# Kernel tuning notes

Measured on AMD Instinct MI355X. Metric: run time of the kernel, lower is better.

Reference implementation:

```python
import jax, jax.numpy as jnp
import numpy as np

D = 1024
HEADS = 16
LN_EPS = 1e-5   # torch LayerNorm default
SHEP_EPS = 1e-4 # eps in shepards_MHA
SHEP_P = 2


def setup_inputs() -> dict:
    key = jax.random.key(0)
    k1, k2, k3 = jax.random.split(key, 3)
    b, t, d = 2, 2048, D
    X = jax.random.normal(k1, (b, t, d), dtype=jnp.float32)
    # Linear weights, scaled like torch default init (~U(-1/sqrt(fan_in), ...)) magnitude
    W_in = jax.random.normal(k2, (4 * d, d), dtype=jnp.float32) * (1.0 / np.sqrt(d))
    b_in = jnp.zeros((4 * d,), dtype=jnp.float32)
    W_out = jax.random.normal(k3, (d, d), dtype=jnp.float32) * (1.0 / np.sqrt(d))
    b_out = jnp.zeros((d,), dtype=jnp.float32)
    return {"X": X, "W_in": W_in, "b_in": b_in, "W_out": W_out, "b_out": b_out}


def _shepards_mha(Q, K, V):
    # Q,K,V: [b,h,t,dh]. Euclidean cdist via ||q||^2 + ||k||^2 - 2 q.k
    q2 = jnp.sum(Q * Q, axis=-1, keepdims=True)          # [b,h,t,1]
    k2 = jnp.sum(K * K, axis=-1, keepdims=True)          # [b,h,t,1]
    sq = q2 + jnp.swapaxes(k2, -1, -2) - 2.0 * jnp.einsum('bhqd,bhkd->bhqk', Q, K)
    dist = jnp.sqrt(jnp.maximum(sq, 0.0))                # [b,h,t,t]
    W = (SHEP_EPS + dist) ** (-SHEP_P)
    W = W / (SHEP_EPS + jnp.sum(W, axis=-1, keepdims=True))
    return jnp.einsum('bhqk,bhkd->bhqd', W, V)


def reference(X, W_in, b_in, W_out, b_out):
    b, t, d = X.shape
    h = HEADS
    dh = d // h
    # LayerNorm (no affine)
    mu = jnp.mean(X, axis=-1, keepdims=True)
    var = jnp.mean((X - mu) ** 2, axis=-1, keepdims=True)
    Xn = (X - mu) / jnp.sqrt(var + LN_EPS)
    # project_in: [b,t,4d]
    P = jnp.einsum('btd,ed->bte', Xn, W_in) + b_in
    # [b,t,h,4*dh] -> [b,h,t,4*dh]
    P = P.reshape(b, t, h, 4 * dh).transpose(0, 2, 1, 3)
    Q, K, V, G = jnp.split(P, 4, axis=-1)                # each [b,h,t,dh]
    A = _shepards_mha(Q, K, V)
    O = (G * A).transpose(0, 2, 1, 3).reshape(b, t, d)
    return X + jnp.einsum('btd,ed->bte', O, W_out) + b_out
```

## Files before the change

kernel.cpp:

```cpp
#include <hip/hip_runtime.h>

#define SEQ 2048
#define D_MODEL 1024
#define NTOK 4096
#define PROW 4096
#define DH 64
#define LN_EPS 1e-5f
#define SHEP_EPS 1e-4f

typedef __attribute__((ext_vector_type(8))) short bf16x8;
typedef __attribute__((ext_vector_type(4))) short s16x4;
typedef __attribute__((ext_vector_type(4))) float f32x4;

__device__ __forceinline__ unsigned short f2bf(float f) {
  union { float f; unsigned u; } v; v.f = f;
  unsigned r = v.u + 0x7fffu + ((v.u >> 16) & 1u);
  return (unsigned short)(r >> 16);
}
__device__ __forceinline__ float bf2f(unsigned short s) {
  union { unsigned u; float f; } v; v.u = ((unsigned)s) << 16;
  return v.f;
}
__device__ __forceinline__ void gload16(const void* g, void* l) {
  __builtin_amdgcn_global_load_lds(
      (const __attribute__((address_space(1))) unsigned int*)g,
      (__attribute__((address_space(3))) unsigned int*)l, 16, 0, 0);
}
__device__ __forceinline__ void gload4(const void* g, void* l) {
  __builtin_amdgcn_global_load_lds(
      (const __attribute__((address_space(1))) unsigned int*)g,
      (__attribute__((address_space(3))) unsigned int*)l, 4, 0, 0);
}
__device__ __forceinline__ unsigned cvt_pk_bf16(float lo, float hi) {
  unsigned r;
  asm("v_cvt_pk_bf16_f32 %0, %1, %2" : "=v"(r) : "v"(lo), "v"(hi));
  return r;
}
#define MFMA16(a, b, c) __builtin_amdgcn_mfma_f32_16x16x32_bf16(a, b, c, 0, 0, 0)

__global__ __launch_bounds__(256) void ln_kernel(const float* __restrict__ X,
                                                 unsigned short* __restrict__ Xn) {
  int row = blockIdx.x, tid = threadIdx.x;
  const float4* xr = (const float4*)(X + (size_t)row * D_MODEL);
  float4 v = xr[tid];
  float s = v.x + v.y + v.z + v.w;
  float s2 = v.x * v.x + v.y * v.y + v.z * v.z + v.w * v.w;
#pragma unroll
  for (int off = 32; off > 0; off >>= 1) {
    s += __shfl_down(s, off);
    s2 += __shfl_down(s2, off);
  }
  __shared__ float red[8];
  __shared__ float mb[2];
  int wv = tid >> 6;
  if ((tid & 63) == 0) { red[wv] = s; red[4 + wv] = s2; }
  __syncthreads();
  if (tid == 0) {
    float ts = red[0] + red[1] + red[2] + red[3];
    float t2 = red[4] + red[5] + red[6] + red[7];
    float mu = ts * (1.f / D_MODEL);
    float var = t2 * (1.f / D_MODEL) - mu * mu;
    mb[0] = mu;
    mb[1] = rsqrtf(var + LN_EPS);
  }
  __syncthreads();
  float mu = mb[0], rs = mb[1];
  s16x4 o;
  o[0] = (short)f2bf((v.x - mu) * rs);
  o[1] = (short)f2bf((v.y - mu) * rs);
  o[2] = (short)f2bf((v.z - mu) * rs);
  o[3] = (short)f2bf((v.w - mu) * rs);
  ((s16x4*)(Xn + (size_t)row * D_MODEL))[tid] = o;
}

__global__ __launch_bounds__(256) void cvt_bf16_kernel(const float* __restrict__ in,
                                                       unsigned short* __restrict__ out,
                                                       int n4) {
  int i = blockIdx.x * 256 + threadIdx.x;
  if (i >= n4) return;
  float4 v = ((const float4*)in)[i];
  s16x4 o;
  o[0] = (short)f2bf(v.x);
  o[1] = (short)f2bf(v.y);
  o[2] = (short)f2bf(v.z);
  o[3] = (short)f2bf(v.w);
  ((s16x4*)out)[i] = o;
}

__global__ __launch_bounds__(256) void gemm_p_kernel(
    const unsigned short* __restrict__ A, const unsigned short* __restrict__ B,
    const float* __restrict__ bias, unsigned short* __restrict__ C,
    int M, int N, int K) {
  __shared__ __align__(16) unsigned short sA[128 * 32];
  __shared__ __align__(16) unsigned short sB[128 * 32];
  int tid = threadIdx.x;
  int m0 = blockIdx.y * 128, n0 = blockIdx.x * 128;
  int wv = tid >> 6, lane = tid & 63;
  int wr = wv >> 1, wc = wv & 1;
  int lr = lane & 15, lq = lane >> 4;
  f32x4 acc[4][4] = {};
  int srow = tid >> 2, scol = (tid & 3) * 8;
  const unsigned short* gA = A + (size_t)(m0 + srow) * K + scol;
  const unsigned short* gB = B + (size_t)(n0 + srow) * K + scol;
  unsigned short* lA = sA + tid * 8;
  unsigned short* lB = sB + tid * 8;
  for (int k0 = 0; k0 < K; k0 += 32) {
    gload16(gA + k0, lA);
    gload16(gA + k0 + (size_t)64 * K, lA + 64 * 32);
    gload16(gB + k0, lB);
    gload16(gB + k0 + (size_t)64 * K, lB + 64 * 32);
    __syncthreads();
    bf16x8 af[4], bfr[4];
#pragma unroll
    for (int m = 0; m < 4; m++)
      af[m] = *(const bf16x8*)&sA[(wr * 64 + m * 16 + lr) * 32 + lq * 8];
#pragma unroll
    for (int n = 0; n < 4; n++)
      bfr[n] = *(const bf16x8*)&sB[(wc * 64 + n * 16 + lr) * 32 + lq * 8];
#pragma unroll
    for (int m = 0; m < 4; m++)
#pragma unroll
      for (int n = 0; n < 4; n++)
        acc[m][n] = MFMA16(af[m], bfr[n], acc[m][n]);
    __syncthreads();
  }
#pragma unroll
  for (int m = 0; m < 4; m++) {
    int row = m0 + wr * 64 + m * 16 + lq * 4;
#pragma unroll
    for (int n = 0; n < 4; n++) {
      int col = n0 + wc * 64 + n * 16 + lr;
      float bv = bias[col];
#pragma unroll
      for (int r = 0; r < 4; r++)
        C[(size_t)(row + r) * N + col] = f2bf(acc[m][n][r] + bv);
    }
  }
}

__global__ __launch_bounds__(256) void gemm_out_kernel(
    const unsigned short* __restrict__ A, const unsigned short* __restrict__ B,
    const float* __restrict__ bias, const float* __restrict__ Xres,
    float* __restrict__ Out, int M, int N, int K) {
  __shared__ __align__(16) unsigned short sA[128 * 32];
  __shared__ __align__(16) unsigned short sB[128 * 32];
  int tid = threadIdx.x;
  int m0 = blockIdx.y * 128, n0 = blockIdx.x * 128;
  int wv = tid >> 6, lane = tid & 63;
  int wr = wv >> 1, wc = wv & 1;
  int lr = lane & 15, lq = lane >> 4;
  f32x4 acc[4][4] = {};
  int srow = tid >> 2, scol = (tid & 3) * 8;
  const unsigned short* gA = A + (size_t)(m0 + srow) * K + scol;
  const unsigned short* gB = B + (size_t)(n0 + srow) * K + scol;
  unsigned short* lA = sA + tid * 8;
  unsigned short* lB = sB + tid * 8;
  for (int k0 = 0; k0 < K; k0 += 32) {
    gload16(gA + k0, lA);
    gload16(gA + k0 + (size_t)64 * K, lA + 64 * 32);
    gload16(gB + k0, lB);
    gload16(gB + k0 + (size_t)64 * K, lB + 64 * 32);
    __syncthreads();
    bf16x8 af[4], bfr[4];
#pragma unroll
    for (int m = 0; m < 4; m++)
      af[m] = *(const bf16x8*)&sA[(wr * 64 + m * 16 + lr) * 32 + lq * 8];
#pragma unroll
    for (int n = 0; n < 4; n++)
      bfr[n] = *(const bf16x8*)&sB[(wc * 64 + n * 16 + lr) * 32 + lq * 8];
#pragma unroll
    for (int m = 0; m < 4; m++)
#pragma unroll
      for (int n = 0; n < 4; n++)
        acc[m][n] = MFMA16(af[m], bfr[n], acc[m][n]);
    __syncthreads();
  }
#pragma unroll
  for (int m = 0; m < 4; m++) {
    int row = m0 + wr * 64 + m * 16 + lq * 4;
#pragma unroll
    for (int n = 0; n < 4; n++) {
      int col = n0 + wc * 64 + n * 16 + lr;
      float bv = bias[col];
#pragma unroll
      for (int r = 0; r < 4; r++) {
        size_t idx = (size_t)(row + r) * N + col;
        Out[idx] = Xres[idx] + acc[m][n][r] + bv;
      }
    }
  }
}

__global__ __launch_bounds__(256) void transv_kernel(const unsigned short* __restrict__ P,
                                                     unsigned short* __restrict__ Vt) {
  int kt = blockIdx.x;
  int bh = blockIdx.y;
  int b = bh >> 4, h = bh & 15;
  __shared__ unsigned short sT[64][72];
  int tid = threadIdx.x;
  const unsigned short* vbase = P + ((size_t)(b * SEQ + kt * 64)) * PROW + h * 256 + 128;
#pragma unroll
  for (int it = 0; it < 2; it++) {
    int c = tid + it * 256;
    int k = c >> 3, c0 = (c & 7) * 8;
    uint4 u = *(const uint4*)(vbase + (size_t)k * PROW + c0);
    unsigned e[4] = {u.x, u.y, u.z, u.w};
#pragma unroll
    for (int j = 0; j < 4; j++) {
      sT[c0 + 2 * j][k] = (unsigned short)(e[j] & 0xffffu);
      sT[c0 + 2 * j + 1][k] = (unsigned short)(e[j] >> 16);
    }
  }
  __syncthreads();
  unsigned short* obase = Vt + (size_t)bh * 64 * SEQ + kt * 64;
#pragma unroll
  for (int it = 0; it < 2; it++) {
    int cc = tid + it * 256;
    int crow = cc >> 3, k0 = (cc & 7) * 8;
    uint4 o;
    unsigned short e[8];
#pragma unroll
    for (int j = 0; j < 8; j++) e[j] = sT[crow][k0 + j];
    o.x = (unsigned)e[0] | ((unsigned)e[1] << 16);
    o.y = (unsigned)e[2] | ((unsigned)e[3] << 16);
    o.z = (unsigned)e[4] | ((unsigned)e[5] << 16);
    o.w = (unsigned)e[6] | ((unsigned)e[7] << 16);
    *(uint4*)(obase + (size_t)crow * SEQ + k0) = o;
  }
}

__global__ __launch_bounds__(256) void norms_kernel(const unsigned short* __restrict__ P,
                                                    float* __restrict__ nrm) {
  int id = blockIdx.x * 256 + threadIdx.x;
  int bh = id >> 12;
  int which = (id >> 11) & 1;
  int t = id & 2047;
  int b = bh >> 4, h = bh & 15;
  const unsigned short* p = P + ((size_t)(b * SEQ + t)) * PROW + h * 256 + which * 64;
  const uint4* pv = (const uint4*)p;
  float acc = 0.f;
#pragma unroll
  for (int i = 0; i < 8; i++) {
    uint4 u = pv[i];
    unsigned arr[4] = {u.x, u.y, u.z, u.w};
#pragma unroll
    for (int j = 0; j < 4; j++) {
      float lo = __uint_as_float(arr[j] << 16);
      float hi = __uint_as_float(arr[j] & 0xffff0000u);
      acc += lo * lo + hi * hi;
    }
  }
  nrm[(size_t)(bh * 2 + which) * SEQ + t] = acc;
}

__global__ __launch_bounds__(512) void attn_kernel(
    const unsigned short* __restrict__ P, const unsigned short* __restrict__ Vt,
    const float* __restrict__ nrm, unsigned short* __restrict__ O) {
  int qt = blockIdx.x, bh = blockIdx.y;
  int b = bh >> 4, h = bh & 15;
  int tid = threadIdx.x;
  int w = tid >> 6, lane = tid & 63;
  int lr = lane & 15, lq = lane >> 4;

  __shared__ __align__(16) unsigned short sQ[128 * 64];
  __shared__ __align__(16) unsigned short sK[2][64 * 64];
  __shared__ __align__(16) unsigned short sV[2][64 * 64];
  __shared__ __align__(16) unsigned short sW[128 * 64];
  __shared__ __align__(16) float sK2[2][64];
  __shared__ __align__(16) float sDen[8][16];

  const unsigned short* qbase = P + ((size_t)(b * SEQ + qt * 128)) * PROW + h * 256;
  const unsigned short* kbase = P + ((size_t)(b * SEQ)) * PROW + h * 256 + 64;
  const unsigned short* vtb = Vt + (size_t)bh * 64 * SEQ;
  const float* k2base = nrm + (size_t)(bh * 2 + 1) * SEQ;

  int srow = tid >> 3;
  int scol = ((tid & 7) ^ (srow & 7)) * 8;
  const unsigned short* kSrc = kbase + (size_t)srow * PROW + scol;
  const unsigned short* vSrc = vtb + (size_t)srow * SEQ + scol;

#pragma unroll
  for (int it = 0; it < 2; it++) {
    int c = tid + it * 512;
    int row = c >> 3;
    int col = ((c & 7) ^ (row & 7)) * 8;
    gload16(qbase + (size_t)row * PROW + col, (char*)sQ + c * 16);
  }
  gload16(kSrc, (char*)&sK[0][0] + tid * 16);
  gload16(vSrc, (char*)&sV[0][0] + tid * 16);
  if (w == 0) gload4(k2base + lane, (char*)&sK2[0][0] + lane * 4);
  float q2 = nrm[(size_t)(bh * 2) * SEQ + qt * 128 + 16 * w + lr];
  __syncthreads();

  int qrow = 16 * w + lr;
  bf16x8 qf[2];
#pragma unroll
  for (int ks = 0; ks < 2; ks++)
    qf[ks] = *(const bf16x8*)((const char*)sQ + qrow * 128 +
                              ((ks * 64 + lq * 16) ^ ((lr & 7) << 4)));

  f32x4 num[4] = {};
  float den = 0.f;
  char* wrow = (char*)sW + qrow * 128;

  for (int kt = 0; kt < SEQ / 64; kt++) {
    int cur = kt & 1, nxt = cur ^ 1;
    if (kt < SEQ / 64 - 1) {
      gload16(kSrc + (size_t)(kt + 1) * 64 * PROW, (char*)&sK[nxt][0] + tid * 16);
      gload16(vSrc + (size_t)(kt + 1) * 64, (char*)&sV[nxt][0] + tid * 16);
      if (w == 0) gload4(k2base + (kt + 1) * 64 + lane, (char*)&sK2[nxt][0] + lane * 4);
    }

    f32x4 st[4] = {};
#pragma unroll
    for (int fk = 0; fk < 4; fk++) {
      int row = 16 * fk + lr;
      const char* krow = (const char*)&sK[cur][0] + row * 128;
      bf16x8 kf0 = *(const bf16x8*)(krow + ((lq * 16) ^ ((row & 7) << 4)));
      bf16x8 kf1 = *(const bf16x8*)(krow + ((64 + lq * 16) ^ ((row & 7) << 4)));
      st[fk] = MFMA16(kf0, qf[0], st[fk]);
      st[fk] = MFMA16(kf1, qf[1], st[fk]);
    }

#pragma unroll
    for (int fk = 0; fk < 4; fk++) {
      f32x4 k2v = *(const f32x4*)&sK2[cur][16 * fk + 4 * lq];
      float w0 = __builtin_amdgcn_rcpf(fmaxf(fmaf(-2.f, st[fk][0], q2 + k2v[0]), 1e-8f));
      float w1 = __builtin_amdgcn_rcpf(fmaxf(fmaf(-2.f, st[fk][1], q2 + k2v[1]), 1e-8f));
      float w2 = __builtin_amdgcn_rcpf(fmaxf(fmaf(-2.f, st[fk][2], q2 + k2v[2]), 1e-8f));
      float w3 = __builtin_amdgcn_rcpf(fmaxf(fmaf(-2.f, st[fk][3], q2 + k2v[3]), 1e-8f));
      den += (w0 + w1) + (w2 + w3);
      uint2 pp;
      pp.x = cvt_pk_bf16(w0, w1);
      pp.y = cvt_pk_bf16(w2, w3);
      *(uint2*)(wrow + ((32 * fk + 8 * lq) ^ ((lr & 7) << 4))) = pp;
    }

#pragma unroll
    for (int ks = 0; ks < 2; ks++) {
      bf16x8 aw = *(const bf16x8*)(wrow + ((64 * ks + 16 * lq) ^ ((lr & 7) << 4)));
#pragma unroll
      for (int fn = 0; fn < 4; fn++) {
        int row = 16 * fn + lr;
        bf16x8 bv = *(const bf16x8*)((const char*)&sV[cur][0] + row * 128 +
                                     ((64 * ks + 16 * lq) ^ ((row & 7) << 4)));
        num[fn] = MFMA16(aw, bv, num[fn]);
      }
    }
    __syncthreads();
  }

  den += __shfl_xor(den, 16);
  den += __shfl_xor(den, 32);
  if (lq == 0) sDen[w][lr] = den;
  __syncthreads();
  f32x4 dv = *(const f32x4*)&sDen[w][4 * lq];
  f32x4 rdv;
#pragma unroll
  for (int r = 0; r < 4; r++) rdv[r] = __builtin_amdgcn_rcpf(dv[r] + SHEP_EPS);

  const unsigned short* gbase = qbase + 192;
#pragma unroll
  for (int fn = 0; fn < 4; fn++) {
    int c = 16 * fn + lr;
#pragma unroll
    for (int r = 0; r < 4; r++) {
      int ql = 16 * w + 4 * lq + r;
      float g = bf2f(gbase[(size_t)ql * PROW + c]);
      float a = num[fn][r] * rdv[r];
      O[((size_t)(b * SEQ + qt * 128 + ql)) * D_MODEL + h * DH + c] = f2bf(g * a);
    }
  }
}

extern "C" void kernel_launch(void* const* d_in, const int* in_sizes, int n_in,
                              void* d_out, int out_size, void* d_ws, size_t ws_size,
                              hipStream_t stream) {
  const float* X = (const float*)d_in[0];
  const float* W_in = (const float*)d_in[1];
  const float* b_in = (const float*)d_in[2];
  const float* W_out = (const float*)d_in[3];
  const float* b_out = (const float*)d_in[4];
  float* out = (float*)d_out;

  char* ws = (char*)d_ws;
  unsigned short* Xn = (unsigned short*)(ws);
  unsigned short* O = (unsigned short*)(ws);
  unsigned short* Wi = (unsigned short*)(ws + ((size_t)8 << 20));
  unsigned short* Vt = (unsigned short*)(ws + ((size_t)8 << 20));
  unsigned short* Wo = (unsigned short*)(ws + ((size_t)16 << 20));
  unsigned short* P = (unsigned short*)(ws + ((size_t)18 << 20));
  float* nrm = (float*)(ws + ((size_t)50 << 20));

  ln_kernel<<<NTOK, 256, 0, stream>>>(X, Xn);
  cvt_bf16_kernel<<<4096, 256, 0, stream>>>(W_in, Wi, (4096 * 1024) / 4);
  cvt_bf16_kernel<<<1024, 256, 0, stream>>>(W_out, Wo, (1024 * 1024) / 4);
  gemm_p_kernel<<<dim3(32, 32), 256, 0, stream>>>(Xn, Wi, b_in, P, 4096, 4096, 1024);
  transv_kernel<<<dim3(32, 32), 256, 0, stream>>>(P, Vt);
  norms_kernel<<<512, 256, 0, stream>>>(P, nrm);
  attn_kernel<<<dim3(16, 32), 512, 0, stream>>>(P, Vt, nrm, O);
  gemm_out_kernel<<<dim3(8, 32), 256, 0, stream>>>(O, Wo, b_out, X, out, 4096, 1024, 1024);
}
```

Before: 170.8 us.

## Merge weight conversions, add XCD tile swizzle to GEMMs, raise MFMA priority

Merges the two weight bf16 conversion launches into one kernel that writes both weights into one contiguous destination, relying on Wo sitting right after Wi in the workspace. Remaps GEMM workgroup indices with an XCD-aware swizzle so that neighbouring tiles land on the same chiplet and share its L2. Wraps the attention MFMA sections in s_setprio so the matrix-issuing waves get scheduling priority. Together these aim to cut launch overhead and improve cache locality and MFMA issue, with small risk from the workspace layout assumption.

After: 170.3 us. No clear change (-0.3%).

```diff
diff --git a/kernel.cpp b/kernel.cpp
--- a/kernel.cpp
+++ b/kernel.cpp
@@ -37,6 +37,11 @@
   return r;
 }
 #define MFMA16(a, b, c) __builtin_amdgcn_mfma_f32_16x16x32_bf16(a, b, c, 0, 0, 0)
+
+__device__ __forceinline__ int xcd_swizzle(int linear, int nwg) {
+  int cpx = nwg >> 3;
+  return (linear & 7) * cpx + (linear >> 3);
+}
 
 __global__ __launch_bounds__(256) void ln_kernel(const float* __restrict__ X,
                                                  unsigned short* __restrict__ Xn) {
@@ -73,18 +78,20 @@
   ((s16x4*)(Xn + (size_t)row * D_MODEL))[tid] = o;
 }
 
-__global__ __launch_bounds__(256) void cvt_bf16_kernel(const float* __restrict__ in,
-                                                       unsigned short* __restrict__ out,
-                                                       int n4) {
+__global__ __launch_bounds__(256) void cvt_both_kernel(const float* __restrict__ Win,
+                                                       const float* __restrict__ Wout,
+                                                       unsigned short* __restrict__ dst) {
+  const int N1 = (4096 * 1024) / 4;
+  const int N2 = (1024 * 1024) / 4;
   int i = blockIdx.x * 256 + threadIdx.x;
-  if (i >= n4) return;
-  float4 v = ((const float4*)in)[i];
+  if (i >= N1 + N2) return;
+  float4 v = (i < N1) ? ((const float4*)Win)[i] : ((const float4*)Wout)[i - N1];
   s16x4 o;
   o[0] = (short)f2bf(v.x);
   o[1] = (short)f2bf(v.y);
   o[2] = (short)f2bf(v.z);
   o[3] = (short)f2bf(v.w);
-  ((s16x4*)out)[i] = o;
+  ((s16x4*)dst)[i] = o;
 }
 
 __global__ __launch_bounds__(256) void gemm_p_kernel(
@@ -94,7 +101,9 @@
   __shared__ __align__(16) unsigned short sA[128 * 32];
   __shared__ __align__(16) unsigned short sB[128 * 32];
   int tid = threadIdx.x;
-  int m0 = blockIdx.y * 128, n0 = blockIdx.x * 128;
+  int nwg = gridDim.x * gridDim.y;
+  int swz = xcd_swizzle(blockIdx.y * gridDim.x + blockIdx.x, nwg);
+  int m0 = (swz / gridDim.x) * 128, n0 = (swz % gridDim.x) * 128;
   int wv = tid >> 6, lane = tid & 63;
   int wr = wv >> 1, wc = wv & 1;
   int lr = lane & 15, lq = lane >> 4;
@@ -145,7 +154,9 @@
   __shared__ __align__(16) unsigned short sA[128 * 32];
   __shared__ __align__(16) unsigned short sB[128 * 32];
   int tid = threadIdx.x;
-  int m0 = blockIdx.y * 128, n0 = blockIdx.x * 128;
+  int nwg = gridDim.x * gridDim.y;
+  int swz = xcd_swizzle(blockIdx.y * gridDim.x + blockIdx.x, nwg);
+  int m0 = (swz / gridDim.x) * 128, n0 = (swz % gridDim.x) * 128;
   int wv = tid >> 6, lane = tid & 63;
   int wr = wv >> 1, wc = wv & 1;
   int lr = lane & 15, lq = lane >> 4;
@@ -312,6 +323,7 @@
     }
 
     f32x4 st[4] = {};
+    __builtin_amdgcn_s_setprio(1);
 #pragma unroll
     for (int fk = 0; fk < 4; fk++) {
       int row = 16 * fk + lr;
@@ -321,6 +333,7 @@
       st[fk] = MFMA16(kf0, qf[0], st[fk]);
       st[fk] = MFMA16(kf1, qf[1], st[fk]);
     }
+    __builtin_amdgcn_s_setprio(0);
 
 #pragma unroll
     for (int fk = 0; fk < 4; fk++) {
@@ -336,6 +349,7 @@
       *(uint2*)(wrow + ((32 * fk + 8 * lq) ^ ((lr & 7) << 4))) = pp;
     }
 
+    __builtin_amdgcn_s_setprio(1);
 #pragma unroll
     for (int ks = 0; ks < 2; ks++) {
       bf16x8 aw = *(const bf16x8*)(wrow + ((64 * ks + 16 * lq) ^ ((lr & 7) << 4)));
@@ -347,6 +361,7 @@
         num[fn] = MFMA16(aw, bv, num[fn]);
       }
     }
+    __builtin_amdgcn_s_setprio(0);
     __syncthreads();
   }
 
@@ -393,8 +408,7 @@
   float* nrm = (float*)(ws + ((size_t)50 << 20));
 
   ln_kernel<<<NTOK, 256, 0, stream>>>(X, Xn);
-  cvt_bf16_kernel<<<4096, 256, 0, stream>>>(W_in, Wi, (4096 * 1024) / 4);
-  cvt_bf16_kernel<<<1024, 256, 0, stream>>>(W_out, Wo, (1024 * 1024) / 4);
+  cvt_both_kernel<<<5120, 256, 0, stream>>>(W_in, W_out, Wi);
   gemm_p_kernel<<<dim3(32, 32), 256, 0, stream>>>(Xn, Wi, b_in, P, 4096, 4096, 1024);
   transv_kernel<<<dim3(32, 32), 256, 0, stream>>>(P, Vt);
   norms_kernel<<<512, 256, 0, stream>>>(P, nrm);
```
